# Kernel tuning notes

Hardware: AMD Instinct MI355X
Metric: run time of the kernel (lower is better)

The kernel has to match this reference:

```python
import jax, jax.numpy as jnp
import numpy as np

LRELU_ALPHA = 0.2       # LeakyReLU slope (alpha arg of GraphAttentionLayer)
NEG_INF = -9e15         # zero_vec value from the torch code
N1, N2, N3 = 3000, 2500, 2500
IN_F, OUT_F, HEADS = 128, 64, 2


def setup_inputs() -> dict:
    key = jax.random.key(0)
    ks = jax.random.split(key, 13)
    N = N1 + N2 + N3
    h = jax.random.normal(ks[0], (N, IN_F), jnp.float32)
    A1  = jax.random.randint(ks[1],  (N1, N1), 0, 2, jnp.int32)
    A2  = jax.random.randint(ks[2],  (N2, N2), 0, 2, jnp.int32)
    A3  = jax.random.randint(ks[3],  (N3, N3), 0, 2, jnp.int32)
    A12 = jax.random.randint(ks[4],  (N1, N2), 0, 2, jnp.int32)
    A13 = jax.random.randint(ks[5],  (N1, N3), 0, 2, jnp.int32)
    A23 = jax.random.randint(ks[6],  (N2, N3), 0, 2, jnp.int32)
    A21 = jax.random.randint(ks[7],  (N2, N1), 0, 2, jnp.int32)
    A31 = jax.random.randint(ks[8],  (N3, N1), 0, 2, jnp.int32)
    A32 = jax.random.randint(ks[9],  (N3, N2), 0, 2, jnp.int32)
    # per-head GAT parameters (xavier-ish scale)
    Ws = jax.random.normal(ks[10], (HEADS, IN_F, OUT_F), jnp.float32) * 0.12
    a_param = jax.random.normal(ks[11], (HEADS, 2 * OUT_F, 1), jnp.float32) * 0.12
    return dict(h=h, A1=A1, A2=A2, A3=A3, A12=A12, A13=A13, A23=A23,
                A21=A21, A31=A31, A32=A32, Ws=Ws, a_param=a_param)


def reference(h, A1, A2, A3, A12, A13, A23, A21, A31, A32, Ws, a_param):
    n1, n2, n3 = A1.shape[0], A2.shape[0], A3.shape[0]
    # The 9 block assignments in the torch forward tile the full NxN matrix,
    # so they are equivalent to one block-structured mask.
    mask = jnp.block([[A1,  A12, A13],
                      [A21, A2,  A23],
                      [A31, A32, A3]]) > 0          # [N, N] bool

    Wh = jnp.einsum('nf,hfo->hno', h, Ws)           # [H, N, O]
    a1 = a_param[:, :OUT_F, 0]                      # [H, O]
    a2 = a_param[:, OUT_F:, 0]                      # [H, O]
    Wh1 = jnp.einsum('hno,ho->hn', Wh, a1)          # [H, N]
    Wh2 = jnp.einsum('hno,ho->hn', Wh, a2)          # [H, N]
    e = jax.nn.leaky_relu(Wh1[:, :, None] + Wh2[:, None, :], LRELU_ALPHA)  # [H,N,N]
    att = jax.nn.softmax(jnp.where(mask[None], e, NEG_INF), axis=-1)
    # dropout is identity in eval mode
    mid = jnp.einsum('hij,hjo->hio', att, Wh)       # [H, N, O]
    out = jax.nn.elu(mid)                           # concat=True -> elu
    x2 = out.transpose(1, 0, 2).reshape(h.shape[0], -1)  # [N, H*O] head concat

    x3 = jax.nn.log_softmax(x2[n1 + n2:], axis=1)   # group-3 nodes
    x4 = jax.nn.log_softmax(x2[:n1], axis=1)        # group-1 nodes
    x5 = jax.nn.log_softmax(x2[n1:n1 + n2], axis=1) # group-2 nodes
    return (x3, x4, x5)
```

## Files before the change

kernel.cpp:

```cpp
#include <hip/hip_runtime.h>
#include <hip/hip_bf16.h>


#define CN1 3000
#define CN2 2500
#define CN3 2500
#define NTOT 8000
#define INF_ 128
#define OUTF 64
#define LOG2E 1.44269504088896340736f
#define ALPHA 0.2f

typedef __attribute__((ext_vector_type(4))) float f32x4;
typedef __attribute__((ext_vector_type(8))) short short8;
typedef __attribute__((ext_vector_type(4))) int i32x4;
union B16x8 { int4 i4; short8 s8; unsigned int u[4]; };

#if defined(__has_builtin)
#if __has_builtin(__builtin_amdgcn_exp2f)
#define EXP2F(x) __builtin_amdgcn_exp2f(x)
#endif
#endif
#ifndef EXP2F
#define EXP2F(x) exp2f(x)
#endif

__device__ inline float wave_sum(float v) {
  for (int d = 32; d; d >>= 1) v += __shfl_xor(v, d, 64);
  return v;
}

__device__ inline unsigned int pk2(float a, float b) {
  union { __hip_bfloat162 h; unsigned int u; } cv;
  cv.h = __float22bfloat162_rn(make_float2(a, b));
  return cv.u;
}

__device__ inline unsigned int pack2_bf16(float a, float b) {
  unsigned ua = __float_as_uint(a);
  ua = (ua + 0x7FFFu + ((ua >> 16) & 1u)) >> 16;
  unsigned ub = __float_as_uint(b);
  ub = (ub + 0x7FFFu + ((ub >> 16) & 1u)) & 0xFFFF0000u;
  return ub | ua;
}

__global__ __launch_bounds__(256)
void k_pack(const int* __restrict__ A1,  const int* __restrict__ A12, const int* __restrict__ A13,
            const int* __restrict__ A21, const int* __restrict__ A2,  const int* __restrict__ A23,
            const int* __restrict__ A31, const int* __restrict__ A32, const int* __restrict__ A3,
            unsigned int* __restrict__ packed) {
  const int i = blockIdx.x * 4 + (threadIdx.x >> 6);
  const int lane = threadIdx.x & 63;
  const int *r0, *r1, *r2;
  if (i < CN1)            { r0 = A1  + i * CN1;          r1 = A12 + i * CN2;          r2 = A13 + i * CN3; }
  else if (i < CN1 + CN2) { int r = i - CN1;       r0 = A21 + r * CN1; r1 = A2  + r * CN2; r2 = A23 + r * CN3; }
  else                    { int r = i - CN1 - CN2; r0 = A31 + r * CN1; r1 = A32 + r * CN2; r2 = A3  + r * CN3; }
  const i32x4* p0 = (const i32x4*)r0;
  const i32x4* p1 = (const i32x4*)r1;
  const i32x4* p2 = (const i32x4*)r2;
  unsigned int* pkrow = packed + (i >> 4) * 4000 + (i & 15);
  const int sh = 4 * (lane & 7);
  const int w  = lane >> 3;
#pragma unroll
  for (int ib = 0; ib < 4; ++ib) {
    i32x4 v[8];
#pragma unroll
    for (int u = 0; u < 8; ++u) {
      int q = (ib * 8 + u) * 64 + lane;
      q = q < 2000 ? q : 1999;
      const i32x4* src = (q < 750) ? (p0 + q) : (q < 1375) ? (p1 + q - 750) : (p2 + q - 1375);
      v[u] = __builtin_nontemporal_load(src);
    }
#pragma unroll
    for (int u = 0; u < 8; ++u) {
      const int it = ib * 8 + u;
      const bool act = (it * 64 + lane) < 2000;
      unsigned int n = (v[u].x > 0 ? 1u : 0u) | (v[u].y > 0 ? 2u : 0u)
                     | (v[u].z > 0 ? 4u : 0u) | (v[u].w > 0 ? 8u : 0u);
      n = act ? (n << sh) : 0u;
      n |= __shfl_xor(n, 1, 64);
      n |= __shfl_xor(n, 2, 64);
      n |= __shfl_xor(n, 4, 64);
      const int wglob = it * 8 + w;
      if ((lane & 7) == 0 && wglob < 250)
        pkrow[wglob * 16] = n;
    }
  }
}

__global__ void k_wh(const float* __restrict__ hv, const float* __restrict__ Wsv,
                     const float* __restrict__ ap,
                     float* __restrict__ Whf,
                     float* __restrict__ Wh1s,
                     float* __restrict__ Wh2s) {
  const int t = threadIdx.x;
  const int o = t & 63;
  const int n = blockIdx.x * 2 + (t >> 6);
  const float* hrow = hv + n * INF_;
  const float* Ws0 = Wsv + o;
  const float* Ws1 = Wsv + INF_ * OUTF + o;
  float a0a = 0.f, a0b = 0.f, a1a = 0.f, a1b = 0.f;
#pragma unroll 8
  for (int f = 0; f < INF_; f += 2) {
    float h0 = hrow[f], h1 = hrow[f + 1];
    a0a += h0 * Ws0[f * OUTF];
    a0b += h1 * Ws0[(f + 1) * OUTF];
    a1a += h0 * Ws1[f * OUTF];
    a1b += h1 * Ws1[(f + 1) * OUTF];
  }
  float acc0 = a0a + a0b, acc1 = a1a + a1b;
  Whf[(0 * NTOT + n) * OUTF + o] = acc0;
  Whf[(1 * NTOT + n) * OUTF + o] = acc1;
  float s10 = wave_sum(acc0 * ap[o]);
  float s20 = wave_sum(acc0 * ap[OUTF + o]);
  float s11 = wave_sum(acc1 * ap[2 * OUTF + o]);
  float s21 = wave_sum(acc1 * ap[3 * OUTF + o]);
  if (o == 0) {
    Wh1s[n] = s10 * LOG2E;        Wh2s[n] = s20 * LOG2E;
    Wh1s[NTOT + n] = s11 * LOG2E; Wh2s[NTOT + n] = s21 * LOG2E;
  }
}

__global__ void k_m2(const float* __restrict__ Wh2s, float* __restrict__ M2s) {
  const int hd = blockIdx.x;
  float mx = -1e30f;
  for (int i = threadIdx.x; i < NTOT; i += 256)
    mx = fmaxf(mx, Wh2s[hd * NTOT + i]);
  for (int d = 32; d; d >>= 1) mx = fmaxf(mx, __shfl_xor(mx, d, 64));
  __shared__ float red[4];
  if ((threadIdx.x & 63) == 0) red[threadIdx.x >> 6] = mx;
  __syncthreads();
  if (threadIdx.x == 0)
    M2s[hd] = fmaxf(fmaxf(red[0], red[1]), fmaxf(red[2], red[3]));
}

__global__ void k_bpack(const float* __restrict__ Whf, int4* __restrict__ WhB) {
  const int gid = blockIdx.x * 256 + threadIdx.x;
  const int lane = gid & 63;
  const int c = (gid >> 6) & 3;
  const int t = (gid >> 8) % 250;
  const int hd = gid / 64000;
  const int jb = t * 32 + (lane >> 4) * 8;
  const int col = c * 16 + (lane & 15);
  const float* src = Whf + (hd * NTOT + jb) * OUTF + col;
  B16x8 out;
#pragma unroll
  for (int e2 = 0; e2 < 4; ++e2)
    out.u[e2] = pack2_bf16(src[(2 * e2) * OUTF], src[(2 * e2 + 1) * OUTF]);
  WhB[gid] = out.i4;
}

__global__ __launch_bounds__(128)
void k_attn_mfma(const unsigned int* __restrict__ packed,
                 const float* __restrict__ Wh1s, const float* __restrict__ Wh2s,
                 const float* __restrict__ M2s, const int4* __restrict__ WhB,
                 float* __restrict__ partAcc,
                 float* __restrict__ partS)
{
  const int widx = threadIdx.x >> 6;
  const int lane = threadIdx.x & 63;
  const int m = lane & 15;
  const int g = lane >> 4;
  const int kb = g * 8;
  const int rowblk = blockIdx.x;
  const int i = rowblk * 16 + m;
  const int jy = blockIdx.y, njy = gridDim.y;
  const int s = jy * 2 + widx, ns = njy * 2;
  const int t0 = (250 * s) / ns, t1 = (250 * (s + 1)) / ns;

  const unsigned int* pkb = packed + rowblk * 4000 + m;

  const float w1s0 = Wh1s[i],        w1s1 = Wh1s[NTOT + i];
  const float y0 = w1s0 + M2s[0],    y1 = w1s1 + M2s[1];
  const float ci0 = fmaxf(y0, ALPHA * y0), ci1 = fmaxf(y1, ALPHA * y1);
  const float a1c0 = w1s0 - ci0, b1c0 = ALPHA * w1s0 - ci0;
  const float a1c1 = w1s1 - ci1, b1c1 = ALPHA * w1s1 - ci1;
  const float* wh2_0 = Wh2s;
  const float* wh2_1 = Wh2s + NTOT;

  f32x4 a0_0 = {0.f,0.f,0.f,0.f}, a0_1 = a0_0, a0_2 = a0_0, a0_3 = a0_0;
  f32x4 a1_0 = a0_0, a1_1 = a0_0, a1_2 = a0_0, a1_3 = a0_0;
  f32x4 s0v = a0_0, s1v = a0_0;

  B16x8 ones;
#pragma unroll
  for (int e2 = 0; e2 < 4; ++e2) ones.u[e2] = 0x3F803F80u;

  struct Frags { int4 f0[4], f1[4]; float4 w0a, w0b, w1a, w1b; };
  auto load_frags = [&](int t, Frags& F) {
    const int4* bp0 = WhB + t * 256 + lane;
    const int4* bp1 = WhB + (250 + t) * 256 + lane;
#pragma unroll
    for (int c = 0; c < 4; ++c) { F.f0[c] = bp0[c * 64]; F.f1[c] = bp1[c * 64]; }
    const float* w0 = wh2_0 + t * 32 + kb;
    const float* w1 = wh2_1 + t * 32 + kb;
    F.w0a = *(const float4*)w0; F.w0b = *(const float4*)(w0 + 4);
    F.w1a = *(const float4*)w1; F.w1b = *(const float4*)(w1 + 4);
  };

  auto compute = [&](unsigned int mw, const Frags& F) {
    const unsigned bits = (mw >> kb) & 0xffu;
    const float w0v[8] = {F.w0a.x, F.w0a.y, F.w0a.z, F.w0a.w, F.w0b.x, F.w0b.y, F.w0b.z, F.w0b.w};
    const float w1v[8] = {F.w1a.x, F.w1a.y, F.w1a.z, F.w1a.w, F.w1b.x, F.w1b.y, F.w1b.z, F.w1b.w};
    float q0[8], q1[8];
#pragma unroll
    for (int e = 0; e < 8; ++e) {
      bool on = ((bits >> e) & 1u) != 0u;
      float xa0 = a1c0 + w0v[e];
      float xb0 = fmaf(ALPHA, w0v[e], b1c0);
      float p0e = EXP2F(fmaxf(xa0, xb0));
      q0[e] = on ? p0e : 0.f;
      float xa1 = a1c1 + w1v[e];
      float xb1 = fmaf(ALPHA, w1v[e], b1c1);
      float p1e = EXP2F(fmaxf(xa1, xb1));
      q1[e] = on ? p1e : 0.f;
    }
    B16x8 af0, af1;
#pragma unroll
    for (int e2 = 0; e2 < 4; ++e2) {
      af0.u[e2] = pk2(q0[2 * e2], q0[2 * e2 + 1]);
      af1.u[e2] = pk2(q1[2 * e2], q1[2 * e2 + 1]);
    }
    B16x8 b;
    b.i4 = F.f0[0]; a0_0 = __builtin_amdgcn_mfma_f32_16x16x32_bf16(af0.s8, b.s8, a0_0, 0, 0, 0);
    b.i4 = F.f0[1]; a0_1 = __builtin_amdgcn_mfma_f32_16x16x32_bf16(af0.s8, b.s8, a0_1, 0, 0, 0);
    b.i4 = F.f0[2]; a0_2 = __builtin_amdgcn_mfma_f32_16x16x32_bf16(af0.s8, b.s8, a0_2, 0, 0, 0);
    b.i4 = F.f0[3]; a0_3 = __builtin_amdgcn_mfma_f32_16x16x32_bf16(af0.s8, b.s8, a0_3, 0, 0, 0);
    s0v = __builtin_amdgcn_mfma_f32_16x16x32_bf16(af0.s8, ones.s8, s0v, 0, 0, 0);
    b.i4 = F.f1[0]; a1_0 = __builtin_amdgcn_mfma_f32_16x16x32_bf16(af1.s8, b.s8, a1_0, 0, 0, 0);
    b.i4 = F.f1[1]; a1_1 = __builtin_amdgcn_mfma_f32_16x16x32_bf16(af1.s8, b.s8, a1_1, 0, 0, 0);
    b.i4 = F.f1[2]; a1_2 = __builtin_amdgcn_mfma_f32_16x16x32_bf16(af1.s8, b.s8, a1_2, 0, 0, 0);
    b.i4 = F.f1[3]; a1_3 = __builtin_amdgcn_mfma_f32_16x16x32_bf16(af1.s8, b.s8, a1_3, 0, 0, 0);
    s1v = __builtin_amdgcn_mfma_f32_16x16x32_bf16(af1.s8, ones.s8, s1v, 0, 0, 0);
  };

  unsigned int mw0 = pkb[t0 * 16];
  unsigned int mw1 = pkb[min(t0 + 1, t1 - 1) * 16];
  Frags FA, FB;
  load_frags(t0, FA);
  int t = t0;
  for (; t + 1 < t1; t += 2) {
    load_frags(t + 1, FB);
    unsigned int mwa = pkb[min(t + 2, t1 - 1) * 16];
    compute(mw0, FA);
    mw0 = mw1; mw1 = mwa;
    load_frags(min(t + 2, t1 - 1), FA);
    unsigned int mwb = pkb[min(t + 3, t1 - 1) * 16];
    compute(mw0, FB);
    mw0 = mw1; mw1 = mwb;
  }
  if (t < t1) compute(mw0, FA);

  __shared__ f32x4 lds[10][64];
  if (widx == 1) {
    lds[0][lane] = a0_0; lds[1][lane] = a0_1; lds[2][lane] = a0_2; lds[3][lane] = a0_3;
    lds[4][lane] = a1_0; lds[5][lane] = a1_1; lds[6][lane] = a1_2; lds[7][lane] = a1_3;
    lds[8][lane] = s0v;  lds[9][lane] = s1v;
  }
  __syncthreads();
  if (widx == 0) {
    a0_0 += lds[0][lane]; a0_1 += lds[1][lane]; a0_2 += lds[2][lane]; a0_3 += lds[3][lane];
    a1_0 += lds[4][lane]; a1_1 += lds[5][lane]; a1_2 += lds[6][lane]; a1_3 += lds[7][lane];
    s0v  += lds[8][lane]; s1v  += lds[9][lane];

    const int base0 = (jy * 2 + 0) * NTOT + rowblk * 16;
    const int base1 = (jy * 2 + 1) * NTOT + rowblk * 16;
    if (m == 0) {
#pragma unroll
      for (int q = 0; q < 4; ++q) {
        partS[base0 + g * 4 + q] = s0v[q];
        partS[base1 + g * 4 + q] = s1v[q];
      }
    }
    float* o0 = partAcc + base0 * OUTF;
    float* o1 = partAcc + base1 * OUTF;
#pragma unroll
    for (int q = 0; q < 4; ++q) {
      const int row = g * 4 + q;
      o0[row * OUTF +      m] = a0_0[q];
      o0[row * OUTF + 16 + m] = a0_1[q];
      o0[row * OUTF + 32 + m] = a0_2[q];
      o0[row * OUTF + 48 + m] = a0_3[q];
      o1[row * OUTF +      m] = a1_0[q];
      o1[row * OUTF + 16 + m] = a1_1[q];
      o1[row * OUTF + 32 + m] = a1_2[q];
      o1[row * OUTF + 48 + m] = a1_3[q];
    }
  }
}

__global__ void k_final(const float* __restrict__ partAcc, const float* __restrict__ partS,
                        int njy, float* __restrict__ out) {
  const int wave = threadIdx.x >> 6, lane = threadIdx.x & 63;
  const int n = blockIdx.x * 4 + wave;
  float x[2];
#pragma unroll
  for (int hd = 0; hd < 2; ++hd) {
    float a = 0.f, s = 0.f;
    for (int jy = 0; jy < njy; ++jy) {
      a += partAcc[((jy * 2 + hd) * NTOT + n) * OUTF + lane];
      s += partS[(jy * 2 + hd) * NTOT + n];
    }
    float mid = a / s;
    x[hd] = mid > 0.f ? mid : (__expf(mid) - 1.f);
  }
  float mx = fmaxf(x[0], x[1]);
  for (int d = 32; d; d >>= 1) mx = fmaxf(mx, __shfl_xor(mx, d, 64));
  float se = __expf(x[0] - mx) + __expf(x[1] - mx);
  for (int d = 32; d; d >>= 1) se += __shfl_xor(se, d, 64);
  const float lse = mx + __logf(se);
  const int orow = (n >= CN1 + CN2) ? (n - CN1 - CN2) : (n + CN3);
  out[orow * 128 + lane]      = x[0] - lse;
  out[orow * 128 + 64 + lane] = x[1] - lse;
}

__global__ void k_sentinel(float* __restrict__ out, float v) {
  out[blockIdx.x * 256 + threadIdx.x] = v;
}

extern "C" void kernel_launch(void* const* d_in, const int* in_sizes, int n_in,
                              void* d_out, int out_size, void* d_ws, size_t ws_size,
                              hipStream_t stream) {
  float* outf = (float*)d_out;

  static const int EXP[12] = {1024000, 9000000, 6250000, 6250000, 7500000, 7500000,
                              6250000, 7500000, 7500000, 6250000, 16384, 256};
  bool exact = (n_in == 12);
  if (exact) for (int i = 0; i < 12; ++i) if (in_sizes[i] != EXP[i]) { exact = false; break; }

  const size_t FIXED = 64000 + 64000 + 256 + 2048000 + 8000000;
  int njy = 0;
  for (int cand = 8; cand >= 1; cand >>= 1) {
    size_t need = FIXED + (size_t)cand * 64000 + (size_t)cand * 4096000;
    if (ws_size >= need) { njy = cand; break; }
  }
  if (!exact || njy == 0) {
    k_sentinel<<<dim3(4000), dim3(256), 0, stream>>>(outf, -148.0f);
    return;
  }

  const float* h  = (const float*)d_in[0];
  const int* A1  = (const int*)d_in[1];
  const int* A2  = (const int*)d_in[2];
  const int* A3  = (const int*)d_in[3];
  const int* A12 = (const int*)d_in[4];
  const int* A13 = (const int*)d_in[5];
  const int* A23 = (const int*)d_in[6];
  const int* A21 = (const int*)d_in[7];
  const int* A31 = (const int*)d_in[8];
  const int* A32 = (const int*)d_in[9];
  const float* Ws = (const float*)d_in[10];
  const float* ap = (const float*)d_in[11];

  char* w = (char*)d_ws;
  float*        Wh1s    = (float*)(w);
  float*        Wh2s    = (float*)(w + 64000);
  float*        M2s     = (float*)(w + 128000);
  int4*         WhB     = (int4*) (w + 128256);
  unsigned int* packed  = (unsigned int*)(w + 2176256);
  float*        partS   = (float*)(w + 10176256);
  float*        Whf     = (float*)(w + 10176256 + (size_t)njy * 64000);
  float*        partAcc = Whf;

  k_pack     <<<dim3(2000),     dim3(256), 0, stream>>>(A1, A12, A13, A21, A2, A23, A31, A32, A3,
                                                        packed);
  k_wh       <<<dim3(4000),     dim3(128), 0, stream>>>(h, Ws, ap, Whf, Wh1s, Wh2s);
  k_m2       <<<dim3(2),        dim3(256), 0, stream>>>(Wh2s, M2s);
  k_bpack    <<<dim3(500),      dim3(256), 0, stream>>>(Whf, WhB);
  k_attn_mfma<<<dim3(500, njy), dim3(128), 0, stream>>>(packed, Wh1s, Wh2s, M2s, WhB,
                                                        partAcc, partS);
  k_final    <<<dim3(2000),     dim3(256), 0, stream>>>(partAcc, partS, njy, outf);
}
```

Before: 349.0 us.

## Split attention work across waves by head instead of by column range

Each of the two waves in a block now handles one attention head over the block's full column range, instead of both heads over half the columns. This halves per-wave register use for accumulators and fragments and removes the LDS reduction and the __syncthreads at the end. In exchange, each wave runs twice as many loop iterations, and both waves read the same packed mask words, though they now load different WhB and Wh2 data.

```diff
diff --git a/kernel.cpp b/kernel.cpp
--- a/kernel.cpp
+++ b/kernel.cpp
@@ -157,7 +157,7 @@
                  float* __restrict__ partAcc,
                  float* __restrict__ partS)
 {
-  const int widx = threadIdx.x >> 6;
+  const int hd = threadIdx.x >> 6;
   const int lane = threadIdx.x & 63;
   const int m = lane & 15;
   const int g = lane >> 4;
@@ -165,73 +165,55 @@
   const int rowblk = blockIdx.x;
   const int i = rowblk * 16 + m;
   const int jy = blockIdx.y, njy = gridDim.y;
-  const int s = jy * 2 + widx, ns = njy * 2;
-  const int t0 = (250 * s) / ns, t1 = (250 * (s + 1)) / ns;
+  const int t0 = (250 * jy) / njy, t1 = (250 * (jy + 1)) / njy;
 
   const unsigned int* pkb = packed + rowblk * 4000 + m;
 
-  const float w1s0 = Wh1s[i],        w1s1 = Wh1s[NTOT + i];
-  const float y0 = w1s0 + M2s[0],    y1 = w1s1 + M2s[1];
-  const float ci0 = fmaxf(y0, ALPHA * y0), ci1 = fmaxf(y1, ALPHA * y1);
-  const float a1c0 = w1s0 - ci0, b1c0 = ALPHA * w1s0 - ci0;
-  const float a1c1 = w1s1 - ci1, b1c1 = ALPHA * w1s1 - ci1;
-  const float* wh2_0 = Wh2s;
-  const float* wh2_1 = Wh2s + NTOT;
-
-  f32x4 a0_0 = {0.f,0.f,0.f,0.f}, a0_1 = a0_0, a0_2 = a0_0, a0_3 = a0_0;
-  f32x4 a1_0 = a0_0, a1_1 = a0_0, a1_2 = a0_0, a1_3 = a0_0;
-  f32x4 s0v = a0_0, s1v = a0_0;
+  const float w1s = Wh1s[hd * NTOT + i];
+  const float y = w1s + M2s[hd];
+  const float ci = fmaxf(y, ALPHA * y);
+  const float a1c = w1s - ci, b1c = ALPHA * w1s - ci;
+  const float* wh2 = Wh2s + hd * NTOT;
+  const int4* WhBh = WhB + hd * 64000;
+
+  f32x4 a_0 = {0.f,0.f,0.f,0.f}, a_1 = a_0, a_2 = a_0, a_3 = a_0;
+  f32x4 sv = a_0;
 
   B16x8 ones;
 #pragma unroll
   for (int e2 = 0; e2 < 4; ++e2) ones.u[e2] = 0x3F803F80u;
 
-  struct Frags { int4 f0[4], f1[4]; float4 w0a, w0b, w1a, w1b; };
+  struct Frags { int4 f[4]; float4 wa, wb; };
   auto load_frags = [&](int t, Frags& F) {
-    const int4* bp0 = WhB + t * 256 + lane;
-    const int4* bp1 = WhB + (250 + t) * 256 + lane;
-#pragma unroll
-    for (int c = 0; c < 4; ++c) { F.f0[c] = bp0[c * 64]; F.f1[c] = bp1[c * 64]; }
-    const float* w0 = wh2_0 + t * 32 + kb;
-    const float* w1 = wh2_1 + t * 32 + kb;
-    F.w0a = *(const float4*)w0; F.w0b = *(const float4*)(w0 + 4);
-    F.w1a = *(const float4*)w1; F.w1b = *(const float4*)(w1 + 4);
+    const int4* bp = WhBh + t * 256 + lane;
+#pragma unroll
+    for (int c = 0; c < 4; ++c) F.f[c] = bp[c * 64];
+    const float* w0 = wh2 + t * 32 + kb;
+    F.wa = *(const float4*)w0; F.wb = *(const float4*)(w0 + 4);
   };
 
   auto compute = [&](unsigned int mw, const Frags& F) {
     const unsigned bits = (mw >> kb) & 0xffu;
-    const float w0v[8] = {F.w0a.x, F.w0a.y, F.w0a.z, F.w0a.w, F.w0b.x, F.w0b.y, F.w0b.z, F.w0b.w};
-    const float w1v[8] = {F.w1a.x, F.w1a.y, F.w1a.z, F.w1a.w, F.w1b.x, F.w1b.y, F.w1b.z, F.w1b.w};
-    float q0[8], q1[8];
+    const float wv[8] = {F.wa.x, F.wa.y, F.wa.z, F.wa.w, F.wb.x, F.wb.y, F.wb.z, F.wb.w};
+    float q[8];
 #pragma unroll
     for (int e = 0; e < 8; ++e) {
       bool on = ((bits >> e) & 1u) != 0u;
-      float xa0 = a1c0 + w0v[e];
-      float xb0 = fmaf(ALPHA, w0v[e], b1c0);
-      float p0e = EXP2F(fmaxf(xa0, xb0));
-      q0[e] = on ? p0e : 0.f;
-      float xa1 = a1c1 + w1v[e];
-      float xb1 = fmaf(ALPHA, w1v[e], b1c1);
-      float p1e = EXP2F(fmaxf(xa1, xb1));
-      q1[e] = on ? p1e : 0.f;
+      float xa = a1c + wv[e];
+      float xb = fmaf(ALPHA, wv[e], b1c);
+      float pe = EXP2F(fmaxf(xa, xb));
+      q[e] = on ? pe : 0.f;
     }
-    B16x8 af0, af1;
-#pragma unroll
-    for (int e2 = 0; e2 < 4; ++e2) {
-      af0.u[e2] = pk2(q0[2 * e2], q0[2 * e2 + 1]);
-      af1.u[e2] = pk2(q1[2 * e2], q1[2 * e2 + 1]);
-    }
+    B16x8 af;
+#pragma unroll
+    for (int e2 = 0; e2 < 4; ++e2)
+      af.u[e2] = pk2(q[2 * e2], q[2 * e2 + 1]);
     B16x8 b;
-    b.i4 = F.f0[0]; a0_0 = __builtin_amdgcn_mfma_f32_16x16x32_bf16(af0.s8, b.s8, a0_0, 0, 0, 0);
-    b.i4 = F.f0[1]; a0_1 = __builtin_amdgcn_mfma_f32_16x16x32_bf16(af0.s8, b.s8, a0_1, 0, 0, 0);
-    b.i4 = F.f0[2]; a0_2 = __builtin_amdgcn_mfma_f32_16x16x32_bf16(af0.s8, b.s8, a0_2, 0, 0, 0);
-    b.i4 = F.f0[3]; a0_3 = __builtin_amdgcn_mfma_f32_16x16x32_bf16(af0.s8, b.s8, a0_3, 0, 0, 0);
-    s0v = __builtin_amdgcn_mfma_f32_16x16x32_bf16(af0.s8, ones.s8, s0v, 0, 0, 0);
-    b.i4 = F.f1[0]; a1_0 = __builtin_amdgcn_mfma_f32_16x16x32_bf16(af1.s8, b.s8, a1_0, 0, 0, 0);
-    b.i4 = F.f1[1]; a1_1 = __builtin_amdgcn_mfma_f32_16x16x32_bf16(af1.s8, b.s8, a1_1, 0, 0, 0);
-    b.i4 = F.f1[2]; a1_2 = __builtin_amdgcn_mfma_f32_16x16x32_bf16(af1.s8, b.s8, a1_2, 0, 0, 0);
-    b.i4 = F.f1[3]; a1_3 = __builtin_amdgcn_mfma_f32_16x16x32_bf16(af1.s8, b.s8, a1_3, 0, 0, 0);
-    s1v = __builtin_amdgcn_mfma_f32_16x16x32_bf16(af1.s8, ones.s8, s1v, 0, 0, 0);
+    b.i4 = F.f[0]; a_0 = __builtin_amdgcn_mfma_f32_16x16x32_bf16(af.s8, b.s8, a_0, 0, 0, 0);
+    b.i4 = F.f[1]; a_1 = __builtin_amdgcn_mfma_f32_16x16x32_bf16(af.s8, b.s8, a_1, 0, 0, 0);
+    b.i4 = F.f[2]; a_2 = __builtin_amdgcn_mfma_f32_16x16x32_bf16(af.s8, b.s8, a_2, 0, 0, 0);
+    b.i4 = F.f[3]; a_3 = __builtin_amdgcn_mfma_f32_16x16x32_bf16(af.s8, b.s8, a_3, 0, 0, 0);
+    sv = __builtin_amdgcn_mfma_f32_16x16x32_bf16(af.s8, ones.s8, sv, 0, 0, 0);
   };
 
   unsigned int mw0 = pkb[t0 * 16];
@@ -251,41 +233,20 @@
   }
   if (t < t1) compute(mw0, FA);
 
-  __shared__ f32x4 lds[10][64];
-  if (widx == 1) {
-    lds[0][lane] = a0_0; lds[1][lane] = a0_1; lds[2][lane] = a0_2; lds[3][lane] = a0_3;
-    lds[4][lane] = a1_0; lds[5][lane] = a1_1; lds[6][lane] = a1_2; lds[7][lane] = a1_3;
-    lds[8][lane] = s0v;  lds[9][lane] = s1v;
-  }
-  __syncthreads();
-  if (widx == 0) {
-    a0_0 += lds[0][lane]; a0_1 += lds[1][lane]; a0_2 += lds[2][lane]; a0_3 += lds[3][lane];
-    a1_0 += lds[4][lane]; a1_1 += lds[5][lane]; a1_2 += lds[6][lane]; a1_3 += lds[7][lane];
-    s0v  += lds[8][lane]; s1v  += lds[9][lane];
-
-    const int base0 = (jy * 2 + 0) * NTOT + rowblk * 16;
-    const int base1 = (jy * 2 + 1) * NTOT + rowblk * 16;
-    if (m == 0) {
-#pragma unroll
-      for (int q = 0; q < 4; ++q) {
-        partS[base0 + g * 4 + q] = s0v[q];
-        partS[base1 + g * 4 + q] = s1v[q];
-      }
-    }
-    float* o0 = partAcc + base0 * OUTF;
-    float* o1 = partAcc + base1 * OUTF;
-#pragma unroll
-    for (int q = 0; q < 4; ++q) {
-      const int row = g * 4 + q;
-      o0[row * OUTF +      m] = a0_0[q];
-      o0[row * OUTF + 16 + m] = a0_1[q];
-      o0[row * OUTF + 32 + m] = a0_2[q];
-      o0[row * OUTF + 48 + m] = a0_3[q];
-      o1[row * OUTF +      m] = a1_0[q];
-      o1[row * OUTF + 16 + m] = a1_1[q];
-      o1[row * OUTF + 32 + m] = a1_2[q];
-      o1[row * OUTF + 48 + m] = a1_3[q];
-    }
+  const int base = (jy * 2 + hd) * NTOT + rowblk * 16;
+  if (m == 0) {
+#pragma unroll
+    for (int q = 0; q < 4; ++q)
+      partS[base + g * 4 + q] = sv[q];
+  }
+  float* o = partAcc + base * OUTF;
+#pragma unroll
+  for (int q = 0; q < 4; ++q) {
+    const int row = g * 4 + q;
+    o[row * OUTF +      m] = a_0[q];
+    o[row * OUTF + 16 + m] = a_1[q];
+    o[row * OUTF + 32 + m] = a_2[q];
+    o[row * OUTF + 48 + m] = a_3[q];
   }
 }
 
```

Result: faster. 339.7 us (-2.7%).
